# Kernel tuning notes

Measured on AMD Instinct MI355X. Metric: run time of the kernel, lower is better.

Reference implementation:

```python
import jax, jax.numpy as jnp
import numpy as np

LN2 = 0.693147
TARGET_MEAN = 200.0
TARGET_STD = 40.0
BUFFER_SIZE = 1000
TARGET_LOG_MEAN = float(np.log2(TARGET_MEAN))
TARGET_LOG_STD = TARGET_STD / (TARGET_MEAN * LN2)
BLOCK = 33_554_432  # 2**25 pitch frames


def setup_inputs() -> dict:
    key = jax.random.key(0)
    k1, k2 = jax.random.split(key)
    u = jax.random.uniform(k1, (BLOCK,), dtype=jnp.float32)
    unvoiced = jax.random.uniform(k2, (BLOCK,), dtype=jnp.float32) < 0.2
    # realistic F0 range 80-480 Hz, zeros for unvoiced frames
    pitch = jnp.where(unvoiced, 0.0, 80.0 + 400.0 * u)
    return {"pitch_values": pitch}


def reference(pitch_values):
    # State is the freshly-initialized tracker: empty buffer, buffer_idx = 0.
    N = pitch_values.shape[0]
    B = BUFFER_SIZE
    valid = pitch_values > 0
    # log2 of valid pitches (safe for invalid lanes)
    log_p = jnp.log2(jnp.where(valid, pitch_values, 1.0))

    # rank of each valid element among valid elements (scatter order)
    rank = jnp.cumsum(valid.astype(jnp.int32)) - 1          # [N]
    n_valid = jnp.maximum(rank[-1] + 1, 0)
    # dense array of valid log-pitches ordered by rank (unique indices)
    dense_idx = jnp.where(valid, rank, N)                    # N is OOB -> dropped
    dense = jnp.zeros((N,), pitch_values.dtype).at[dense_idx].set(log_p, mode='drop')

    # circular buffer: slot j holds the LAST (max-rank) value written there
    slot = jnp.where(valid, rank % B, B)                     # B is OOB -> dropped
    winner = jnp.full((B,), -1, jnp.int32).at[slot].max(rank, mode='drop')
    filled = winner >= 0
    buf = jnp.where(filled, dense[jnp.clip(winner, 0, N - 1)], 0.0)

    count = jnp.minimum(n_valid, B)
    cnt_f = jnp.maximum(count, 1).astype(pitch_values.dtype)
    mean = jnp.sum(buf) / cnt_f
    mean = jnp.where(count > 0, mean, 0.0)                   # init mean = 0.0
    var = jnp.sum(jnp.where(filled, (buf - mean) ** 2, 0.0)) / jnp.maximum(count - 1, 1).astype(pitch_values.dtype)
    std = jnp.where(count > 1, jnp.sqrt(var), 1.0)           # unbiased std (torch default)
    std = jnp.maximum(std, 1e-7)

    normalized = (log_p - mean) / std
    scaled = normalized * TARGET_LOG_STD + TARGET_LOG_MEAN
    return jnp.where(valid, jnp.exp2(scaled), 0.0)
```

## Files before the change

kernel.cpp:

```cpp
#include <hip/hip_runtime.h>
#include <math.h>

#define BUF_SIZE 1000
#define TARGET_LOG_MEAN 7.6438561897747395f
#define TARGET_LOG_STD  (40.0f / (200.0f * 0.693147f))

__global__ void stats_kernel(const float* __restrict__ pitch, long long n,
                             float* __restrict__ stats) {
    const int tid = threadIdx.x;
    __shared__ int s_cnt[256];
    __shared__ double s_red[256];

    double sum = 0.0, sumsq = 0.0;
    long long count_so_far = 0;

    const long long nchunks = (n + 1023) >> 10;
    for (long long c = nchunks - 1; c >= 0; --c) {
        const long long base = (c << 10) + (long long)tid * 4;
        float v[4];
        int valid[4];
        int cnt = 0;
#pragma unroll
        for (int j = 0; j < 4; ++j) {
            const long long idx = base + j;
            const float p = (idx < n) ? pitch[idx] : 0.0f;
            v[j] = p;
            valid[j] = (p > 0.0f) ? 1 : 0;
            cnt += valid[j];
        }

        s_cnt[tid] = cnt;
        __syncthreads();
        for (int off = 1; off < 256; off <<= 1) {
            const int mine = s_cnt[tid];
            const int add = (tid >= off) ? s_cnt[tid - off] : 0;
            __syncthreads();
            s_cnt[tid] = mine + add;
            __syncthreads();
        }
        const int incl = s_cnt[tid];
        const int total = s_cnt[255];
        const int suff_after = total - incl;

        int r = 0;
#pragma unroll
        for (int j = 3; j >= 0; --j) {
            if (valid[j]) {
                const long long rev = count_so_far + suff_after + r;
                if (rev < BUF_SIZE) {
                    const double lp = (double)__log2f(v[j]);
                    sum += lp;
                    sumsq += lp * lp;
                }
                r++;
            }
        }

        count_so_far += total;
        __syncthreads();
        if (count_so_far >= BUF_SIZE) break;
    }

    s_red[tid] = sum;
    __syncthreads();
    for (int off = 128; off > 0; off >>= 1) {
        if (tid < off) s_red[tid] += s_red[tid + off];
        __syncthreads();
    }
    const double tsum = s_red[0];
    __syncthreads();
    s_red[tid] = sumsq;
    __syncthreads();
    for (int off = 128; off > 0; off >>= 1) {
        if (tid < off) s_red[tid] += s_red[tid + off];
        __syncthreads();
    }
    const double tsumsq = s_red[0];

    if (tid == 0) {
        const long long count = (count_so_far < BUF_SIZE) ? count_so_far : BUF_SIZE;
        float mean, stdv;
        if (count == 0) {
            mean = 0.0f;
            stdv = 1.0f;
        } else {
            mean = (float)(tsum / (double)count);
            if (count > 1) {
                double var = (tsumsq - tsum * tsum / (double)count) /
                             (double)(count - 1);
                if (var < 0.0) var = 0.0;
                stdv = (float)sqrt(var);
            } else {
                stdv = 1.0f;
            }
        }
        if (stdv < 1e-7f) stdv = 1e-7f;
        const float scale = TARGET_LOG_STD / stdv;
        const float bias = TARGET_LOG_MEAN - mean * scale;
        stats[0] = scale;
        stats[1] = bias;
    }
}

__global__ void apply_kernel(const float4* __restrict__ in4,
                             float4* __restrict__ out4, long long n4,
                             const float* __restrict__ pitch,
                             float* __restrict__ out, long long n,
                             const float* __restrict__ stats) {
    const float scale = stats[0];
    const float bias = stats[1];
    const long long gid = (long long)blockIdx.x * blockDim.x + threadIdx.x;
    const long long stride = (long long)gridDim.x * blockDim.x;

    for (long long k = gid; k < n4; k += stride) {
        const float4 p = in4[k];
        float4 o;
        o.x = (p.x > 0.0f) ? exp2f(fmaf(__log2f(p.x), scale, bias)) : 0.0f;
        o.y = (p.y > 0.0f) ? exp2f(fmaf(__log2f(p.y), scale, bias)) : 0.0f;
        o.z = (p.z > 0.0f) ? exp2f(fmaf(__log2f(p.z), scale, bias)) : 0.0f;
        o.w = (p.w > 0.0f) ? exp2f(fmaf(__log2f(p.w), scale, bias)) : 0.0f;
        out4[k] = o;
    }

    const long long tail_start = n4 * 4;
    for (long long k = tail_start + gid; k < n; k += stride) {
        const float p = pitch[k];
        out[k] = (p > 0.0f) ? exp2f(fmaf(__log2f(p), scale, bias)) : 0.0f;
    }
}

extern "C" void kernel_launch(void* const* d_in, const int* in_sizes, int n_in,
                              void* d_out, int out_size, void* d_ws, size_t ws_size,
                              hipStream_t stream) {
    const float* pitch = (const float*)d_in[0];
    float* out = (float*)d_out;
    const long long n = (long long)in_sizes[0];
    float* stats = (float*)d_ws;

    stats_kernel<<<1, 256, 0, stream>>>(pitch, n, stats);

    const long long n4 = n / 4;
    int blocks = (int)((n4 + 255) / 256);
    if (blocks > 32768) blocks = 32768;
    if (blocks < 1) blocks = 1;
    apply_kernel<<<blocks, 256, 0, stream>>>((const float4*)pitch, (float4*)out,
                                             n4, pitch, out, n, stats);
}
```

Measured before the change: 225.3 us.

## Fuse stats and apply kernels, recomputing stats redundantly per block

Merges the single-block stats kernel and the elementwise apply kernel into one launch. Every block recomputes the buffer statistics from the tail of the input, keeps scale and bias in shared memory, then runs a grid-stride apply loop. The grid is capped at 2048 blocks instead of 32768. This drops a kernel launch and the serial dependency on a global stats write, at the cost of duplicating the small tail scan in every block.

Measured after the change: 235.3 us. 1.04x slower.

```diff
diff --git a/kernel.cpp b/kernel.cpp
--- a/kernel.cpp
+++ b/kernel.cpp
@@ -5,11 +5,12 @@
 #define TARGET_LOG_MEAN 7.6438561897747395f
 #define TARGET_LOG_STD  (40.0f / (200.0f * 0.693147f))
 
-__global__ void stats_kernel(const float* __restrict__ pitch, long long n,
-                             float* __restrict__ stats) {
+__global__ void fused_kernel(const float* __restrict__ pitch, long long n,
+                             float* __restrict__ out) {
     const int tid = threadIdx.x;
     __shared__ int s_cnt[256];
     __shared__ double s_red[256];
+    __shared__ float s_sb[2];
 
     double sum = 0.0, sumsq = 0.0;
     long long count_so_far = 0;
@@ -96,21 +97,19 @@
         }
         if (stdv < 1e-7f) stdv = 1e-7f;
         const float scale = TARGET_LOG_STD / stdv;
-        const float bias = TARGET_LOG_MEAN - mean * scale;
-        stats[0] = scale;
-        stats[1] = bias;
+        s_sb[0] = scale;
+        s_sb[1] = TARGET_LOG_MEAN - mean * scale;
     }
-}
+    __syncthreads();
 
-__global__ void apply_kernel(const float4* __restrict__ in4,
-                             float4* __restrict__ out4, long long n4,
-                             const float* __restrict__ pitch,
-                             float* __restrict__ out, long long n,
-                             const float* __restrict__ stats) {
-    const float scale = stats[0];
-    const float bias = stats[1];
-    const long long gid = (long long)blockIdx.x * blockDim.x + threadIdx.x;
+    const float scale = s_sb[0];
+    const float bias = s_sb[1];
+
+    const long long n4 = n >> 2;
+    const long long gid = (long long)blockIdx.x * blockDim.x + tid;
     const long long stride = (long long)gridDim.x * blockDim.x;
+    const float4* in4 = (const float4*)pitch;
+    float4* out4 = (float4*)out;
 
     for (long long k = gid; k < n4; k += stride) {
         const float4 p = in4[k];
@@ -122,7 +121,7 @@
         out4[k] = o;
     }
 
-    const long long tail_start = n4 * 4;
+    const long long tail_start = n4 << 2;
     for (long long k = tail_start + gid; k < n; k += stride) {
         const float p = pitch[k];
         out[k] = (p > 0.0f) ? exp2f(fmaf(__log2f(p), scale, bias)) : 0.0f;
@@ -135,14 +134,11 @@
     const float* pitch = (const float*)d_in[0];
     float* out = (float*)d_out;
     const long long n = (long long)in_sizes[0];
-    float* stats = (float*)d_ws;
 
-    stats_kernel<<<1, 256, 0, stream>>>(pitch, n, stats);
+    int blocks = 2048;
+    const long long n4 = n >> 2;
+    const long long needed = (n4 + 255) / 256;
+    if ((long long)blocks > needed) blocks = (int)(needed > 0 ? needed : 1);
 
-    const long long n4 = n / 4;
-    int blocks = (int)((n4 + 255) / 256);
-    if (blocks > 32768) blocks = 32768;
-    if (blocks < 1) blocks = 1;
-    apply_kernel<<<blocks, 256, 0, stream>>>((const float4*)pitch, (float4*)out,
-                                             n4, pitch, out, n, stats);
+    fused_kernel<<<blocks, 256, 0, stream>>>(pitch, n, out);
 }
```
